# Optimization experiments

Hardware: AMD Instinct MI355X
Metric: run time of the kernel (lower is better)

The kernel has to match this reference:

```python
import jax, jax.numpy as jnp
import numpy as np

D = 1024
H = 16
HD = D // H
DFF = 4 * D
B, L = 2, 2048
EPS = 1e-5


def setup_inputs() -> dict:
    key = jax.random.key(0)
    ks = jax.random.split(key, 12)
    s = lambda fan_in: 1.0 / np.sqrt(fan_in)
    inp = {
        "x": jax.random.normal(ks[0], (B, L, D), jnp.float32),
        "mask": jnp.ones((1, 1, L, L), jnp.bool_),
        "ln_g": jnp.ones((D,), jnp.float32),
        "ln_b": jnp.zeros((D,), jnp.float32),
        "qkv_w": jax.random.uniform(ks[1], (3 * D, D), jnp.float32, -s(D), s(D)),
        "qkv_b": jax.random.uniform(ks[2], (3 * D,), jnp.float32, -s(D), s(D)),
        "wo_w": jax.random.uniform(ks[3], (D, D), jnp.float32, -s(D), s(D)),
        "wo_b": jax.random.uniform(ks[4], (D,), jnp.float32, -s(D), s(D)),
        "m0_w": jax.random.uniform(ks[5], (DFF, D), jnp.float32, -s(D), s(D)),
        "m0_b": jax.random.uniform(ks[6], (DFF,), jnp.float32, -s(D), s(D)),
        "m1_w": jax.random.uniform(ks[7], (D, DFF), jnp.float32, -s(DFF), s(DFF)),
        "m1_b": jax.random.uniform(ks[8], (D,), jnp.float32, -s(DFF), s(DFF)),
    }
    return inp


def _layer_norm(x, g, b):
    mu = jnp.mean(x, axis=-1, keepdims=True)
    var = jnp.var(x, axis=-1, keepdims=True)
    return (x - mu) * jax.lax.rsqrt(var + EPS) * g + b


def reference(x, mask, ln_g, ln_b, qkv_w, qkv_b, wo_w, wo_b, m0_w, m0_b, m1_w, m1_b):
    b, l, d = x.shape
    # --- pre-norm self-attention ---
    xn = _layer_norm(x, ln_g, ln_b)
    qkv = xn @ qkv_w.T + qkv_b                       # [B, L, 3D]
    qkv = qkv.reshape(b, l, 3, H, HD).transpose(2, 0, 3, 1, 4)  # [3, B, H, L, HD]
    q, k, v = qkv[0], qkv[1], qkv[2]
    scores = jnp.einsum("bhld,bhmd->bhlm", q, k) / np.sqrt(HD)  # [B, H, L, L]
    scores = jnp.where(mask, scores, -1e9)
    attn = jax.nn.softmax(scores, axis=-1)
    ctx = jnp.einsum("bhlm,bhmd->bhld", attn, v)     # [B, H, L, HD]
    ctx = ctx.transpose(0, 2, 1, 3).reshape(b, l, d)
    x = x + ctx @ wo_w.T + wo_b
    # --- GELU MLP (same shared LayerNorm params) ---
    xn = _layer_norm(x, ln_g, ln_b)
    h = jax.nn.gelu(xn @ m0_w.T + m0_b, approximate=False)
    return x + h @ m1_w.T + m1_b
```

## Files before the change

kernel.cpp:

```cpp
#include <hip/hip_runtime.h>
#include <hip/hip_bf16.h>
#include <math.h>

#define BL 4096
#define DM 1024
#define NH 16
#define HD 64
#define DFF 4096
#define SEQ 2048
#define EPS 1e-5f
#define QSCALE 0.18033688011112042f

typedef __bf16 bf16x8 __attribute__((ext_vector_type(8)));
typedef float f32x4 __attribute__((ext_vector_type(4)));
typedef float f32x16 __attribute__((ext_vector_type(16)));

__device__ __forceinline__ unsigned short f2bf(float f) {
    __hip_bfloat16 h = __float2bfloat16(f);
    return *reinterpret_cast<unsigned short*>(&h);
}

__device__ __forceinline__ unsigned int pack2bf(float p0, float p1) {
    unsigned int u0 = __builtin_bit_cast(unsigned int, p0) + 0x8000u;
    unsigned int u1 = __builtin_bit_cast(unsigned int, p1) + 0x8000u;
    return __builtin_amdgcn_perm(u1, u0, 0x07060302);
}

__device__ __forceinline__ void gload_lds16(const void* g, void* l) {
    __builtin_amdgcn_global_load_lds(
        (const __attribute__((address_space(1))) unsigned int*)g,
        (__attribute__((address_space(3))) unsigned int*)l,
        16, 0, 0);
}

__global__ __launch_bounds__(256)
void f2b4_kernel(const float* __restrict__ s0, const float* __restrict__ s1,
                 const float* __restrict__ s2, const float* __restrict__ s3,
                 unsigned short* __restrict__ d0, unsigned short* __restrict__ d1,
                 unsigned short* __restrict__ d2, unsigned short* __restrict__ d3,
                 int n0, int n1, int n2, int n3) {
    int i = blockIdx.x * 256 + threadIdx.x;
    const float* s; unsigned short* d; int j = i;
    if (j < n0) { s = s0; d = d0; }
    else if ((j -= n0) < n1) { s = s1; d = d1; }
    else if ((j -= n1) < n2) { s = s2; d = d2; }
    else if ((j -= n2) < n3) { s = s3; d = d3; }
    else return;
    float4 v = ((const float4*)s)[j];
    ushort4 o = {f2bf(v.x), f2bf(v.y), f2bf(v.z), f2bf(v.w)};
    ((ushort4*)d)[j] = o;
}

__global__ __launch_bounds__(256)
void ln_kernel(const float* __restrict__ x, const float* __restrict__ g,
               const float* __restrict__ b, unsigned short* __restrict__ o) {
    int row = blockIdx.x;
    int tid = threadIdx.x;
    const float* xr = x + (size_t)row * DM;
    float4 v = *(const float4*)(xr + tid * 4);
    float s  = v.x + v.y + v.z + v.w;
    float ss = v.x*v.x + v.y*v.y + v.z*v.z + v.w*v.w;
    #pragma unroll
    for (int off = 32; off > 0; off >>= 1) {
        s  += __shfl_down(s, off);
        ss += __shfl_down(ss, off);
    }
    __shared__ float ps[4], pss[4];
    __shared__ float sh_mu, sh_rs;
    int wid = tid >> 6, lane = tid & 63;
    if (lane == 0) { ps[wid] = s; pss[wid] = ss; }
    __syncthreads();
    if (tid == 0) {
        float S = ps[0] + ps[1] + ps[2] + ps[3];
        float SS = pss[0] + pss[1] + pss[2] + pss[3];
        float mu = S * (1.0f / DM);
        float var = SS * (1.0f / DM) - mu * mu;
        sh_mu = mu;
        sh_rs = 1.0f / sqrtf(var + EPS);
    }
    __syncthreads();
    float mu = sh_mu, rs = sh_rs;
    float4 gv = *(const float4*)(g + tid * 4);
    float4 bv = *(const float4*)(b + tid * 4);
    ushort4 ov;
    ov.x = f2bf((v.x - mu) * rs * gv.x + bv.x);
    ov.y = f2bf((v.y - mu) * rs * gv.y + bv.y);
    ov.z = f2bf((v.z - mu) * rs * gv.z + bv.z);
    ov.w = f2bf((v.w - mu) * rs * gv.w + bv.w);
    *(ushort4*)(o + (size_t)row * DM + tid * 4) = ov;
}

template <int EPI, int TN, int BK, int KSPLIT, typename OUT_T>
__global__ __launch_bounds__(256)
void gemm_bt_mfma(const unsigned short* __restrict__ A,
                  const unsigned short* __restrict__ B,
                  const float* __restrict__ bias, const float* __restrict__ res,
                  OUT_T* __restrict__ C, int M, int N, int K,
                  unsigned short* __restrict__ vt) {
    constexpr int RPC = 512 / BK;
    constexpr int CA  = 128 / RPC;
    constexpr int CB  = TN / RPC;
    constexpr int FJ  = TN / 32;
    __shared__ unsigned short As[128 * BK];
    __shared__ unsigned short Bs[TN * BK];
    const int tid = threadIdx.x, lane = tid & 63, wave = tid >> 6;

    const int id   = blockIdx.x;
    const int xcd  = id & 7, slot = id >> 3;
    const int R    = (M / 128) >> 3;
    const int by   = xcd * R + (slot % R);
    const int bx   = slot / R;
    const int m0 = by * 128, n0 = bx * TN;
    const int wm = (wave >> 1) * 64, wn = (wave & 1) * (TN / 2);
    const int k0 = blockIdx.y * (K / KSPLIT);

    const int srow = (BK == 32) ? (lane >> 2) : (lane >> 3);
    const int scol = (BK == 32) ? (lane & 3) * 8
                                : ((lane & 7) ^ (srow & 7)) * 8;
    const int fr = lane & 15;
    const int g  = lane >> 4;

    f32x4 acc[4][FJ] = {};

    for (int kt = k0; kt < k0 + K / KSPLIT; kt += BK) {
        __syncthreads();
        #pragma unroll
        for (int ci = 0; ci < (CA + CB) / 4; ci++) {
            const int c = ci * 4 + wave;
            if (c < CA)
                gload_lds16(A + (size_t)(m0 + c * RPC + srow) * K + kt + scol,
                            (char*)As + c * 1024);
            else
                gload_lds16(B + (size_t)(n0 + (c - CA) * RPC + srow) * K + kt + scol,
                            (char*)Bs + (c - CA) * 1024);
        }
        __syncthreads();

        #pragma unroll
        for (int ko = 0; ko < BK / 32; ko++) {
            const int col = (BK == 32) ? (ko * 32 + g * 8)
                                       : (((ko * 4 + g) ^ (fr & 7)) * 8);
            bf16x8 af[4], bfv[FJ];
            #pragma unroll
            for (int i = 0; i < 4; i++)
                af[i] = *(const bf16x8*)(As + (wm + i * 16 + fr) * BK + col);
            #pragma unroll
            for (int j = 0; j < FJ; j++)
                bfv[j] = *(const bf16x8*)(Bs + (wn + j * 16 + fr) * BK + col);
            #pragma unroll
            for (int i = 0; i < 4; i++)
                #pragma unroll
                for (int j = 0; j < FJ; j++)
                    acc[i][j] = __builtin_amdgcn_mfma_f32_16x16x32_bf16(af[i], bfv[j], acc[i][j], 0, 0, 0);
        }
    }

    const int col  = lane & 15;
    const int rowq = (lane >> 4) * 4;
    const bool kz0 = (KSPLIT == 1) || (blockIdx.y == 0);
    float bs[FJ];
    #pragma unroll
    for (int j = 0; j < FJ; j++) bs[j] = bias[n0 + wn + j * 16 + col];
    #pragma unroll
    for (int i = 0; i < 4; i++) {
        #pragma unroll
        for (int r = 0; r < 4; r++) {
            const size_t row = (size_t)(m0 + wm + i * 16 + rowq + r);
            #pragma unroll
            for (int j = 0; j < FJ; j++) {
                const int c = n0 + wn + j * 16 + col;
                const size_t off = row * N + c;
                float v = acc[i][j][r];
                if (EPI != 4) v += bs[j];
                if (EPI == 1) v += res[off];
                if (EPI == 2) {
                    float u = v * (0.7978845608028654f + 0.035677408136300125f * v * v);
                    float e = __builtin_amdgcn_exp2f(u * 2.885390081777927f);
                    float th = 1.0f - 2.0f * __builtin_amdgcn_rcpf(e + 1.0f);
                    v = 0.5f * v * (1.0f + th);
                }
                if (EPI == 3) {
                    if (c < 2048) {
                        float vq = (c < 1024) ? v * QSCALE : v;
                        ((unsigned short*)C)[off] = f2bf(vq);
                    } else {
                        int d = c & 63, hh = (c >> 6) & 15;
                        int bb = (int)(row >> 11), l = (int)(row & 2047);
                        vt[((size_t)((bb * 16 + hh) * 64 + d)) * 2048 + l] = f2bf(v);
                    }
                } else if (EPI == 4) {
                    if (kz0) v += bs[j];
                    unsafeAtomicAdd((float*)C + off, v);
                } else if constexpr (sizeof(OUT_T) == 2) {
                    ((unsigned short*)C)[off] = f2bf(v);
                } else {
                    ((float*)C)[off] = v;
                }
            }
        }
    }
}

__global__ __launch_bounds__(256)
void attn_mfma(const unsigned short* __restrict__ qkv,
               const unsigned short* __restrict__ vt,
               unsigned short* __restrict__ ctx) {
    __shared__ unsigned short Ks[128 * 64];
    __shared__ unsigned short Vts[2][64 * 64];
    const int bid = blockIdx.x;
    const int xcd = bid & 7, sl = bid >> 3;
    const int qt = sl & 15, pg = sl >> 4;
    const int pair = pg * 8 + xcd;
    const int h = pair & 15, b = pair >> 4;
    const int tid = threadIdx.x, lane = tid & 63, wave = tid >> 6;
    const int hh = lane >> 5, mm = lane & 31;
    const int q0 = b * 2048 + qt * 128 + wave * 32;

    bf16x8 qf[4];
    const unsigned short* qb = qkv + (size_t)(q0 + mm) * 3072 + h * 64 + hh * 8;
    #pragma unroll
    for (int s = 0; s < 4; s++) qf[s] = *(const bf16x8*)(qb + s * 16);

    const int skey = lane >> 3;
    const int sgr  = (lane & 7) ^ (skey & 7);
    const unsigned short* kbase = qkv + ((size_t)(b * 2048) + skey) * 3072 + 1024 + h * 64 + sgr * 8;
    const unsigned short* vbase = vt + ((size_t)((b * 16 + h) * 64) + skey) * 2048 + sgr * 8;

    float l_lane = 0.0f;
    f32x16 o_acc[2] = {};

    for (int kt = 0; kt < SEQ; kt += 128) {
        __syncthreads();
        #pragma unroll
        for (int rep = 0; rep < 4; rep++) {
            int c = rep * 4 + wave;
            gload_lds16(kbase + (size_t)(kt + c * 8) * 3072, (char*)Ks + c * 1024);
        }
        #pragma unroll
        for (int rep = 0; rep < 2; rep++) {
            int c = rep * 4 + wave;
            gload_lds16(vbase + (size_t)(c * 8) * 2048 + kt,      (char*)Vts[0] + c * 1024);
            gload_lds16(vbase + (size_t)(c * 8) * 2048 + kt + 64, (char*)Vts[1] + c * 1024);
        }
        __syncthreads();

        #pragma unroll
        for (int sub = 0; sub < 2; sub++) {
            f32x16 sT[2] = {};
            #pragma unroll
            for (int t = 0; t < 2; t++)
                #pragma unroll
                for (int s = 0; s < 4; s++) {
                    bf16x8 kf = *(const bf16x8*)(Ks + (sub * 64 + t * 32 + mm) * 64 + ((s * 2 + hh) ^ (mm & 7)) * 8);
                    sT[t] = __builtin_amdgcn_mfma_f32_32x32x16_bf16(kf, qf[s], sT[t], 0, 0, 0);
                }

            unsigned int pk[2][8];
            #pragma unroll
            for (int t = 0; t < 2; t++)
                #pragma unroll
                for (int e = 0; e < 8; e++) {
                    float p0 = __builtin_amdgcn_exp2f(sT[t][2 * e]);
                    float p1 = __builtin_amdgcn_exp2f(sT[t][2 * e + 1]);
                    l_lane += p0 + p1;
                    pk[t][e] = pack2bf(p0, p1);
                }

            #pragma unroll
            for (int w = 0; w < 4; w++) {
                const int t = w >> 1, eb = (w & 1) * 4;
                unsigned int sx = hh ? pk[t][eb + 0] : pk[t][eb + 2];
                unsigned int sy = hh ? pk[t][eb + 1] : pk[t][eb + 3];
                unsigned int rx = (unsigned int)__shfl_xor((int)sx, 32);
                unsigned int ry = (unsigned int)__shfl_xor((int)sy, 32);
                union { unsigned int u[4]; bf16x8 v; } af;
                af.u[0] = hh ? rx : pk[t][eb + 0];
                af.u[1] = hh ? ry : pk[t][eb + 1];
                af.u[2] = hh ? pk[t][eb + 2] : rx;
                af.u[3] = hh ? pk[t][eb + 3] : ry;
                #pragma unroll
                for (int dt = 0; dt < 2; dt++) {
                    bf16x8 vf = *(const bf16x8*)(Vts[sub] + (dt * 32 + mm) * 64 + ((w * 2 + hh) ^ (mm & 7)) * 8);
                    o_acc[dt] = __builtin_amdgcn_mfma_f32_32x32x16_bf16(af.v, vf, o_acc[dt], 0, 0, 0);
                }
            }
        }
    }

    float inv_own = 1.0f / (l_lane + __shfl_xor(l_lane, 32));
    #pragma unroll
    for (int r = 0; r < 16; r++) {
        const int rowq = (r & 3) + 8 * (r >> 2) + 4 * hh;
        float inv = __shfl(inv_own, rowq);
        size_t base = (size_t)(q0 + rowq) * 1024 + h * 64 + mm;
        ctx[base]      = f2bf(o_acc[0][r] * inv);
        ctx[base + 32] = f2bf(o_acc[1][r] * inv);
    }
}

extern "C" void kernel_launch(void* const* d_in, const int* in_sizes, int n_in,
                              void* d_out, int out_size, void* d_ws, size_t ws_size,
                              hipStream_t stream) {
    const float* x     = (const float*)d_in[0];
    const float* ln_g  = (const float*)d_in[2];
    const float* ln_b  = (const float*)d_in[3];
    const float* qkv_w = (const float*)d_in[4];
    const float* qkv_b = (const float*)d_in[5];
    const float* wo_w  = (const float*)d_in[6];
    const float* wo_b  = (const float*)d_in[7];
    const float* m0_w  = (const float*)d_in[8];
    const float* m0_b  = (const float*)d_in[9];
    const float* m1_w  = (const float*)d_in[10];
    const float* m1_b  = (const float*)d_in[11];
    float* out = (float*)d_out;

    char* ws = (char*)d_ws;
    unsigned short* xn_bf  = (unsigned short*)(ws);
    unsigned short* qkv_bf = (unsigned short*)(ws + (size_t)8  * 1024 * 1024);
    unsigned short* vt_bf  = (unsigned short*)(ws + (size_t)32 * 1024 * 1024);
    unsigned short* ctx_bf = (unsigned short*)(ws + (size_t)40 * 1024 * 1024);
    unsigned short* h_bf   = (unsigned short*)(ws + (size_t)48 * 1024 * 1024);
    unsigned short* qkvw_b = (unsigned short*)(ws + (size_t)80 * 1024 * 1024);
    unsigned short* wow_b  = (unsigned short*)(ws + (size_t)86 * 1024 * 1024);
    unsigned short* m0w_b  = (unsigned short*)(ws + (size_t)88 * 1024 * 1024);
    unsigned short* m1w_b  = (unsigned short*)(ws + (size_t)96 * 1024 * 1024);

    {
        int n0 = 3 * DM * DM / 4, n1 = DM * DM / 4, n2 = DFF * DM / 4, n3 = DM * DFF / 4;
        int tot = n0 + n1 + n2 + n3;
        f2b4_kernel<<<(tot + 255) / 256, 256, 0, stream>>>(
            qkv_w, wo_w, m0_w, m1_w, qkvw_b, wow_b, m0w_b, m1w_b, n0, n1, n2, n3);
    }

    ln_kernel<<<BL, 256, 0, stream>>>(x, ln_g, ln_b, xn_bf);
    gemm_bt_mfma<3, 128, 32, 1, unsigned short><<<(3072 / 128) * (BL / 128), 256, 0, stream>>>(
        xn_bf, qkvw_b, qkv_b, nullptr, qkv_bf, BL, 3072, DM, vt_bf);
    attn_mfma<<<2 * NH * (SEQ / 128), 256, 0, stream>>>(qkv_bf, vt_bf, ctx_bf);
    gemm_bt_mfma<1, 64, 32, 1, float><<<(DM / 64) * (BL / 128), 256, 0, stream>>>(
        ctx_bf, wow_b, wo_b, x, out, BL, DM, DM, nullptr);
    ln_kernel<<<BL, 256, 0, stream>>>(out, ln_g, ln_b, xn_bf);
    gemm_bt_mfma<2, 128, 32, 1, unsigned short><<<(DFF / 128) * (BL / 128), 256, 0, stream>>>(
        xn_bf, m0w_b, m0_b, nullptr, h_bf, BL, DFF, DM, nullptr);
    gemm_bt_mfma<4, 64, 64, 2, float><<<dim3((DM / 64) * (BL / 128), 2), 256, 0, stream>>>(
        h_bf, m1w_b, m1_b, nullptr, out, BL, DM, DFF, nullptr);
}
```

Baseline: 374.3 us.

## Widen GEMM K-tiles with swizzled LDS, stage V-transpose through LDS, drop split-K atomics

All GEMMs now use larger K tiles (64, or 128 for the down projection) with an XOR-swizzled LDS layout for every tile width. The V part of the QKV projection is transposed through shared memory and written as coalesced 16-byte stores, replacing scattered 2-byte writes. The split-K atomic down projection becomes a single-pass residual epilogue that reads and writes out in place. Together these aim to cut syncs per K step, uncoalesced stores and atomic traffic, at the cost of more LDS per block and possibly lower occupancy or parallelism for the last GEMM.

Measured after the change: 355.1 us. -5.1%, faster.

```diff
diff --git a/kernel.cpp b/kernel.cpp
--- a/kernel.cpp
+++ b/kernel.cpp
@@ -90,7 +90,7 @@
     *(ushort4*)(o + (size_t)row * DM + tid * 4) = ov;
 }
 
-template <int EPI, int TN, int BK, int KSPLIT, typename OUT_T>
+template <int EPI, int TN, int BK, typename OUT_T>
 __global__ __launch_bounds__(256)
 void gemm_bt_mfma(const unsigned short* __restrict__ A,
                   const unsigned short* __restrict__ B,
@@ -101,8 +101,9 @@
     constexpr int CA  = 128 / RPC;
     constexpr int CB  = TN / RPC;
     constexpr int FJ  = TN / 32;
-    __shared__ unsigned short As[128 * BK];
-    __shared__ unsigned short Bs[TN * BK];
+    __shared__ unsigned short smem[(128 + TN) * BK];
+    unsigned short* As = smem;
+    unsigned short* Bs = smem + 128 * BK;
     const int tid = threadIdx.x, lane = tid & 63, wave = tid >> 6;
 
     const int id   = blockIdx.x;
@@ -112,34 +113,32 @@
     const int bx   = slot / R;
     const int m0 = by * 128, n0 = bx * TN;
     const int wm = (wave >> 1) * 64, wn = (wave & 1) * (TN / 2);
-    const int k0 = blockIdx.y * (K / KSPLIT);
-
-    const int srow = (BK == 32) ? (lane >> 2) : (lane >> 3);
-    const int scol = (BK == 32) ? (lane & 3) * 8
-                                : ((lane & 7) ^ (srow & 7)) * 8;
+
+    const int srow  = (BK == 64) ? (lane >> 3) : (lane >> 4);
+    const int sslot = (BK == 64) ? (lane & 7)  : (lane & 15);
     const int fr = lane & 15;
     const int g  = lane >> 4;
 
     f32x4 acc[4][FJ] = {};
 
-    for (int kt = k0; kt < k0 + K / KSPLIT; kt += BK) {
+    for (int kt = 0; kt < K; kt += BK) {
         __syncthreads();
         #pragma unroll
         for (int ci = 0; ci < (CA + CB) / 4; ci++) {
             const int c = ci * 4 + wave;
-            if (c < CA)
-                gload_lds16(A + (size_t)(m0 + c * RPC + srow) * K + kt + scol,
-                            (char*)As + c * 1024);
-            else
-                gload_lds16(B + (size_t)(n0 + (c - CA) * RPC + srow) * K + kt + scol,
-                            (char*)Bs + (c - CA) * 1024);
+            const bool isA = (c < CA);
+            const int cc = isA ? c : c - CA;
+            const int cr = cc * RPC + srow;
+            const unsigned short* src = (isA ? A + (size_t)(m0 + cr) * K
+                                             : B + (size_t)(n0 + cr) * K)
+                                        + kt + ((sslot ^ (cr & 7)) * 8);
+            gload_lds16(src, (char*)(isA ? As : Bs) + cc * 1024);
         }
         __syncthreads();
 
         #pragma unroll
         for (int ko = 0; ko < BK / 32; ko++) {
-            const int col = (BK == 32) ? (ko * 32 + g * 8)
-                                       : (((ko * 4 + g) ^ (fr & 7)) * 8);
+            const int col = (((ko * 4 + g) ^ (fr & 7)) * 8);
             bf16x8 af[4], bfv[FJ];
             #pragma unroll
             for (int i = 0; i < 4; i++)
@@ -157,10 +156,41 @@
 
     const int col  = lane & 15;
     const int rowq = (lane >> 4) * 4;
-    const bool kz0 = (KSPLIT == 1) || (blockIdx.y == 0);
     float bs[FJ];
     #pragma unroll
     for (int j = 0; j < FJ; j++) bs[j] = bias[n0 + wn + j * 16 + col];
+
+    if (EPI == 3 && n0 >= 2048) {
+        __syncthreads();
+        #pragma unroll
+        for (int i = 0; i < 4; i++) {
+            const int l0 = wm + i * 16 + rowq;
+            #pragma unroll
+            for (int j = 0; j < FJ; j++) {
+                const int dcol = wn + j * 16 + col;
+                float v0 = acc[i][j][0] + bs[j], v1 = acc[i][j][1] + bs[j];
+                float v2 = acc[i][j][2] + bs[j], v3 = acc[i][j][3] + bs[j];
+                uint2 pk = {pack2bf(v0, v1), pack2bf(v2, v3)};
+                char* p = (char*)smem + dcol * 256 +
+                          (((l0 >> 3) ^ (dcol & 7)) * 16) + (l0 & 7) * 2;
+                *(uint2*)p = pk;
+            }
+        }
+        __syncthreads();
+        const int bb = m0 >> 11, lbase = m0 & 2047;
+        #pragma unroll
+        for (int k = 0; k < 8; k++) {
+            const int oid = tid + k * 256;
+            const int dcol = oid >> 4, lc = oid & 15;
+            uint4 val = *(const uint4*)((const char*)smem + dcol * 256 +
+                                        ((lc ^ (dcol & 7)) * 16));
+            const int c = n0 + dcol;
+            const int d = c & 63, hh2 = (c >> 6) & 15;
+            *(uint4*)(vt + ((size_t)((bb * 16 + hh2) * 64 + d)) * 2048 + lbase + lc * 8) = val;
+        }
+        return;
+    }
+
     #pragma unroll
     for (int i = 0; i < 4; i++) {
         #pragma unroll
@@ -170,8 +200,7 @@
             for (int j = 0; j < FJ; j++) {
                 const int c = n0 + wn + j * 16 + col;
                 const size_t off = row * N + c;
-                float v = acc[i][j][r];
-                if (EPI != 4) v += bs[j];
+                float v = acc[i][j][r] + bs[j];
                 if (EPI == 1) v += res[off];
                 if (EPI == 2) {
                     float u = v * (0.7978845608028654f + 0.035677408136300125f * v * v);
@@ -180,17 +209,8 @@
                     v = 0.5f * v * (1.0f + th);
                 }
                 if (EPI == 3) {
-                    if (c < 2048) {
-                        float vq = (c < 1024) ? v * QSCALE : v;
-                        ((unsigned short*)C)[off] = f2bf(vq);
-                    } else {
-                        int d = c & 63, hh = (c >> 6) & 15;
-                        int bb = (int)(row >> 11), l = (int)(row & 2047);
-                        vt[((size_t)((bb * 16 + hh) * 64 + d)) * 2048 + l] = f2bf(v);
-                    }
-                } else if (EPI == 4) {
-                    if (kz0) v += bs[j];
-                    unsafeAtomicAdd((float*)C + off, v);
+                    float vq = (c < 1024) ? v * QSCALE : v;
+                    ((unsigned short*)C)[off] = f2bf(vq);
                 } else if constexpr (sizeof(OUT_T) == 2) {
                     ((unsigned short*)C)[off] = f2bf(v);
                 } else {
@@ -333,14 +353,14 @@
     }
 
     ln_kernel<<<BL, 256, 0, stream>>>(x, ln_g, ln_b, xn_bf);
-    gemm_bt_mfma<3, 128, 32, 1, unsigned short><<<(3072 / 128) * (BL / 128), 256, 0, stream>>>(
+    gemm_bt_mfma<3, 128, 64, unsigned short><<<(3072 / 128) * (BL / 128), 256, 0, stream>>>(
         xn_bf, qkvw_b, qkv_b, nullptr, qkv_bf, BL, 3072, DM, vt_bf);
     attn_mfma<<<2 * NH * (SEQ / 128), 256, 0, stream>>>(qkv_bf, vt_bf, ctx_bf);
-    gemm_bt_mfma<1, 64, 32, 1, float><<<(DM / 64) * (BL / 128), 256, 0, stream>>>(
+    gemm_bt_mfma<1, 64, 64, float><<<(DM / 64) * (BL / 128), 256, 0, stream>>>(
         ctx_bf, wow_b, wo_b, x, out, BL, DM, DM, nullptr);
     ln_kernel<<<BL, 256, 0, stream>>>(out, ln_g, ln_b, xn_bf);
-    gemm_bt_mfma<2, 128, 32, 1, unsigned short><<<(DFF / 128) * (BL / 128), 256, 0, stream>>>(
+    gemm_bt_mfma<2, 128, 64, unsigned short><<<(DFF / 128) * (BL / 128), 256, 0, stream>>>(
         xn_bf, m0w_b, m0_b, nullptr, h_bf, BL, DFF, DM, nullptr);
-    gemm_bt_mfma<4, 64, 64, 2, float><<<dim3((DM / 64) * (BL / 128), 2), 256, 0, stream>>>(
-        h_bf, m1w_b, m1_b, nullptr, out, BL, DM, DFF, nullptr);
-}
+    gemm_bt_mfma<1, 64, 128, float><<<(DM / 64) * (BL / 128), 256, 0, stream>>>(
+        h_bf, m1w_b, m1_b, out, out, BL, DM, DFF, nullptr);
+}
```
